# Kernel tuning notes

Hardware: AMD Instinct MI355X
Metric: run time of the kernel (lower is better)

Reference implementation:

```python
import jax, jax.numpy as jnp
import numpy as np

N_NODES = 50000
N_EDGES = 800000
F_IN = 64
F_OUT = 64


def setup_inputs() -> dict:
    key = jax.random.key(0)
    k1, k2, k3, k4, k5 = jax.random.split(key, 5)
    x = jax.random.normal(k1, (N_NODES, F_IN), dtype=jnp.float32)
    edge_index = jax.random.randint(k2, (2, N_EDGES), 0, N_NODES, dtype=jnp.int32)
    # PyG GraphConv params: lin_rel (with bias) applied to aggregated neighbors,
    # lin_root (no bias) applied to the node's own features.
    scale = 1.0 / np.sqrt(F_IN)
    W_rel = jax.random.uniform(k3, (F_OUT, F_IN), dtype=jnp.float32, minval=-scale, maxval=scale)
    b_rel = jax.random.uniform(k4, (F_OUT,), dtype=jnp.float32, minval=-scale, maxval=scale)
    W_root = jax.random.uniform(k5, (F_OUT, F_IN), dtype=jnp.float32, minval=-scale, maxval=scale)
    return {"x": x, "W_rel": W_rel, "b_rel": b_rel, "W_root": W_root, "edge_index": edge_index}


def reference(x, W_rel, b_rel, W_root, edge_index):
    # GraphConv (aggr='add'): out = lin_rel(sum_{j in N(i)} x_j) + lin_root(x_i), then ReLU
    src, dst = edge_index[0], edge_index[1]
    # gather neighbor features along edges, scatter-add into destination nodes
    agg = jax.ops.segment_sum(x[src], dst, num_segments=x.shape[0])  # [N, F_IN]
    out = agg @ W_rel.T + b_rel + x @ W_root.T  # [N, F_OUT]
    return jax.nn.relu(out)
```

## Files before the change

### kernel.cpp

```cpp
#include <hip/hip_runtime.h>


#define FD 64
#define TN 64
#define BC 2048
#define KP 65
#define CS 16
#define TM 1024
#define GB 512

__global__ __launch_bounds__(256) void gcv4_prep(
    const float* __restrict__ W_rel, const float* __restrict__ W_root,
    float* __restrict__ WTrel, float* __restrict__ WTroot,
    int* __restrict__ tcnt, int n_cnt) {
  const int idx = blockIdx.x * 256 + threadIdx.x;
  if (idx < FD * FD) {
    const int o = idx >> 6, k = idx & 63;
    WTrel[k * FD + o] = W_rel[idx];
    WTroot[k * FD + o] = W_root[idx];
  }
  for (int i = idx; i < n_cnt; i += gridDim.x * 256) tcnt[i] = 0;
}

__global__ __launch_bounds__(256) void gcv4_bin(
    const int* __restrict__ eidx, int* __restrict__ tcnt,
    unsigned* __restrict__ tbuf, int n_edges, int n_tiles) {
  __shared__ int hcnt[TM];
  __shared__ int hbase[TM];

  const int t = threadIdx.x;
  for (int i = t; i < n_tiles; i += 256) hcnt[i] = 0;
  __syncthreads();

  const int per = (n_edges + gridDim.x - 1) / gridDim.x;
  const int e0 = blockIdx.x * per;
  const int e1 = min(e0 + per, n_edges);

  for (int e = e0 + t; e < e1; e += 256)
    atomicAdd(&hcnt[eidx[n_edges + e] >> 6], 1);
  __syncthreads();

  for (int i = t; i < n_tiles; i += 256) {
    const int c = hcnt[i];
    hbase[i] = (c > 0) ? atomicAdd(&tcnt[i * CS], c) : 0;
    hcnt[i] = 0;
  }
  __syncthreads();

  for (int e = e0 + t; e < e1; e += 256) {
    const int s = eidx[e];
    const int d = eidx[n_edges + e];
    const int tl = d >> 6;
    const int p = hbase[tl] + atomicAdd(&hcnt[tl], 1);
    if (p < BC)
      tbuf[(size_t)tl * BC + p] = ((unsigned)d << 16) | (unsigned)s;
  }
}

__global__ __launch_bounds__(256) void gcv4_main(
    const float* __restrict__ x,
    const float* __restrict__ WTrel,
    const float* __restrict__ b_rel,
    const float* __restrict__ WTroot,
    const int* __restrict__ tcnt,
    const unsigned* __restrict__ tbuf,
    float* __restrict__ out, int n_nodes) {
  __shared__ float aggT[FD * KP];
  __shared__ unsigned short sl[BC + 64];
  __shared__ int hh[TN];
  __shared__ int oo[TN + 1];
  __shared__ int cc[TN];

  const int t = threadIdx.x;
  const int lane = t & 63;
  const int w = t >> 6;
  const int tile = blockIdx.x;
  const int node0 = tile * TN;
  const int cnt = min(tcnt[tile * CS], BC);
  const unsigned* lst = tbuf + (size_t)tile * BC;

  if (t < TN) hh[t] = 0;
  if (t < 64 && cnt + t < BC + 64) sl[cnt + t] = 0;
  __syncthreads();

  for (int i = t; i < cnt; i += 256) atomicAdd(&hh[(lst[i] >> 16) & 63], 1);
  __syncthreads();

  if (w == 0) {
    int v = hh[lane];
    int s = v;
#pragma unroll
    for (int d = 1; d < 64; d <<= 1) {
      int u = __shfl_up(s, d, 64);
      if (lane >= d) s += u;
    }
    oo[lane] = s - v;
    cc[lane] = s - v;
    if (lane == 63) oo[64] = s;
  }
  __syncthreads();

  for (int i = t; i < cnt; i += 256) {
    const unsigned e = lst[i];
    const int d = (int)((e >> 16) & 63);
    sl[atomicAdd(&cc[d], 1)] = (unsigned short)(e & 0xFFFFu);
  }
  __syncthreads();

  const int slot = lane >> 4;
  const int fq = lane & 15;
  for (int nn = 0; nn < 16; ++nn) {
    const int d = w * 16 + nn;
    const int jb = oo[d];
    const int je = oo[d + 1];
    float4 acc = make_float4(0.f, 0.f, 0.f, 0.f);
    const int i0 = slot, i1 = 4 + slot, i2 = 8 + slot, i3 = 12 + slot;
    for (int e0 = jb; e0 < je; e0 += 16) {
      const int m = je - e0;
      const int j0 = (i0 < m) ? e0 + i0 : cnt;
      const int j1 = (i1 < m) ? e0 + i1 : cnt;
      const int j2 = (i2 < m) ? e0 + i2 : cnt;
      const int j3 = (i3 < m) ? e0 + i3 : cnt;
      const int s0 = (int)sl[j0];
      const int s1 = (int)sl[j1];
      const int s2 = (int)sl[j2];
      const int s3 = (int)sl[j3];
      const float4 f0 = *(const float4*)(x + (size_t)s0 * FD + fq * 4);
      const float4 f1 = *(const float4*)(x + (size_t)s1 * FD + fq * 4);
      const float4 f2 = *(const float4*)(x + (size_t)s2 * FD + fq * 4);
      const float4 f3 = *(const float4*)(x + (size_t)s3 * FD + fq * 4);
      acc.x += (i0 < m ? f0.x : 0.f); acc.y += (i0 < m ? f0.y : 0.f);
      acc.z += (i0 < m ? f0.z : 0.f); acc.w += (i0 < m ? f0.w : 0.f);
      acc.x += (i1 < m ? f1.x : 0.f); acc.y += (i1 < m ? f1.y : 0.f);
      acc.z += (i1 < m ? f1.z : 0.f); acc.w += (i1 < m ? f1.w : 0.f);
      acc.x += (i2 < m ? f2.x : 0.f); acc.y += (i2 < m ? f2.y : 0.f);
      acc.z += (i2 < m ? f2.z : 0.f); acc.w += (i2 < m ? f2.w : 0.f);
      acc.x += (i3 < m ? f3.x : 0.f); acc.y += (i3 < m ? f3.y : 0.f);
      acc.z += (i3 < m ? f3.z : 0.f); acc.w += (i3 < m ? f3.w : 0.f);
    }
    acc.x += __shfl_xor(acc.x, 16, 64); acc.y += __shfl_xor(acc.y, 16, 64);
    acc.z += __shfl_xor(acc.z, 16, 64); acc.w += __shfl_xor(acc.w, 16, 64);
    acc.x += __shfl_xor(acc.x, 32, 64); acc.y += __shfl_xor(acc.y, 32, 64);
    acc.z += __shfl_xor(acc.z, 32, 64); acc.w += __shfl_xor(acc.w, 32, 64);
    if (slot == 0) {
      aggT[(fq * 4 + 0) * KP + d] = acc.x;
      aggT[(fq * 4 + 1) * KP + d] = acc.y;
      aggT[(fq * 4 + 2) * KP + d] = acc.z;
      aggT[(fq * 4 + 3) * KP + d] = acc.w;
    }
  }
  __syncthreads();

  const int oq = t & 15, rq = t >> 4;
  const int o0 = oq * 4, r0 = rq * 4;
  const float* xp0 = x + (size_t)min(node0 + r0 + 0, n_nodes - 1) * FD;
  const float* xp1 = x + (size_t)min(node0 + r0 + 1, n_nodes - 1) * FD;
  const float* xp2 = x + (size_t)min(node0 + r0 + 2, n_nodes - 1) * FD;
  const float* xp3 = x + (size_t)min(node0 + r0 + 3, n_nodes - 1) * FD;
  const float4 bias = *(const float4*)(b_rel + o0);
  float acc[4][4];
#pragma unroll
  for (int ri = 0; ri < 4; ++ri) {
    acc[ri][0] = bias.x; acc[ri][1] = bias.y;
    acc[ri][2] = bias.z; acc[ri][3] = bias.w;
  }
#pragma unroll 2
  for (int k0 = 0; k0 < FD; k0 += 4) {
    const float4 q0 = *(const float4*)(xp0 + k0);
    const float4 q1 = *(const float4*)(xp1 + k0);
    const float4 q2 = *(const float4*)(xp2 + k0);
    const float4 q3 = *(const float4*)(xp3 + k0);
#pragma unroll
    for (int kk = 0; kk < 4; ++kk) {
      const int k = k0 + kk;
      const float4 wr = *(const float4*)(WTrel + k * FD + o0);
      const float4 wo = *(const float4*)(WTroot + k * FD + o0);
      const float a0 = aggT[k * KP + r0 + 0];
      const float a1 = aggT[k * KP + r0 + 1];
      const float a2 = aggT[k * KP + r0 + 2];
      const float a3 = aggT[k * KP + r0 + 3];
      const float x0 = ((const float*)&q0)[kk];
      const float x1 = ((const float*)&q1)[kk];
      const float x2 = ((const float*)&q2)[kk];
      const float x3 = ((const float*)&q3)[kk];
      acc[0][0] += a0 * wr.x + x0 * wo.x; acc[0][1] += a0 * wr.y + x0 * wo.y;
      acc[0][2] += a0 * wr.z + x0 * wo.z; acc[0][3] += a0 * wr.w + x0 * wo.w;
      acc[1][0] += a1 * wr.x + x1 * wo.x; acc[1][1] += a1 * wr.y + x1 * wo.y;
      acc[1][2] += a1 * wr.z + x1 * wo.z; acc[1][3] += a1 * wr.w + x1 * wo.w;
      acc[2][0] += a2 * wr.x + x2 * wo.x; acc[2][1] += a2 * wr.y + x2 * wo.y;
      acc[2][2] += a2 * wr.z + x2 * wo.z; acc[2][3] += a2 * wr.w + x2 * wo.w;
      acc[3][0] += a3 * wr.x + x3 * wo.x; acc[3][1] += a3 * wr.y + x3 * wo.y;
      acc[3][2] += a3 * wr.z + x3 * wo.z; acc[3][3] += a3 * wr.w + x3 * wo.w;
    }
  }
#pragma unroll
  for (int ri = 0; ri < 4; ++ri) {
    const int gi = node0 + r0 + ri;
    if (gi < n_nodes) {
      float4 o4;
      o4.x = fmaxf(acc[ri][0], 0.f); o4.y = fmaxf(acc[ri][1], 0.f);
      o4.z = fmaxf(acc[ri][2], 0.f); o4.w = fmaxf(acc[ri][3], 0.f);
      *(float4*)(out + (size_t)gi * FD + o0) = o4;
    }
  }
}

extern "C" void kernel_launch(void* const* d_in, const int* in_sizes, int n_in,
                              void* d_out, int out_size, void* d_ws, size_t ws_size,
                              hipStream_t stream) {
  const float* x      = (const float*)d_in[0];
  const float* W_rel  = (const float*)d_in[1];
  const float* b_rel  = (const float*)d_in[2];
  const float* W_root = (const float*)d_in[3];
  const int* eidx     = (const int*)d_in[4];

  const int n_nodes = in_sizes[0] / FD;
  const int n_edges = in_sizes[4] / 2;
  const int n_tiles = (n_nodes + TN - 1) / TN;

  int* tcnt      = (int*)d_ws;
  unsigned* tbuf = (unsigned*)(tcnt + (size_t)n_tiles * CS);
  float* WTrel   = (float*)(tbuf + (size_t)n_tiles * BC);
  float* WTroot  = WTrel + FD * FD;

  float* out = (float*)d_out;

  const int n_cnt = n_tiles * CS;
  const int gPrep = (n_cnt + 255) / 256;
  gcv4_prep<<<gPrep, 256, 0, stream>>>(W_rel, W_root, WTrel, WTroot, tcnt,
                                       n_cnt);

  gcv4_bin<<<GB, 256, 0, stream>>>(eidx, tcnt, tbuf, n_edges, n_tiles);

  gcv4_main<<<n_tiles, 256, 0, stream>>>(x, WTrel, b_rel, WTroot, tcnt, tbuf,
                                         out, n_nodes);
}
```

Baseline: 173.9 us.

## Use 512 threads per tile and stage root features in shared memory

The main kernel's block size doubles to 512 threads, so each wavefront aggregates 8 destination nodes instead of 16 and each thread computes 2 output rows instead of 4. The tile's own x rows are loaded coalesced into a transposed shared-memory buffer at the start, replacing strided per-thread global float4 loads in the dense projection. This raises parallelism per tile and removes redundant global reads of x. The cost is more shared memory per block (an extra 64x65 float array), which may limit how many blocks fit per CU.

After: 162.3 us. 6.7% less time.

```diff
diff --git a/kernel.cpp b/kernel.cpp
--- a/kernel.cpp
+++ b/kernel.cpp
@@ -9,7 +9,7 @@
 #define TM 1024
 #define GB 512
 
-__global__ __launch_bounds__(256) void gcv4_prep(
+__global__ __launch_bounds__(256) void gcv5_prep(
     const float* __restrict__ W_rel, const float* __restrict__ W_root,
     float* __restrict__ WTrel, float* __restrict__ WTroot,
     int* __restrict__ tcnt, int n_cnt) {
@@ -22,7 +22,7 @@
   for (int i = idx; i < n_cnt; i += gridDim.x * 256) tcnt[i] = 0;
 }
 
-__global__ __launch_bounds__(256) void gcv4_bin(
+__global__ __launch_bounds__(256) void gcv5_bin(
     const int* __restrict__ eidx, int* __restrict__ tcnt,
     unsigned* __restrict__ tbuf, int n_edges, int n_tiles) {
   __shared__ int hcnt[TM];
@@ -57,7 +57,7 @@
   }
 }
 
-__global__ __launch_bounds__(256) void gcv4_main(
+__global__ __launch_bounds__(512) void gcv5_main(
     const float* __restrict__ x,
     const float* __restrict__ WTrel,
     const float* __restrict__ b_rel,
@@ -66,6 +66,7 @@
     const unsigned* __restrict__ tbuf,
     float* __restrict__ out, int n_nodes) {
   __shared__ float aggT[FD * KP];
+  __shared__ float xT[FD * KP];
   __shared__ unsigned short sl[BC + 64];
   __shared__ int hh[TN];
   __shared__ int oo[TN + 1];
@@ -81,9 +82,24 @@
 
   if (t < TN) hh[t] = 0;
   if (t < 64 && cnt + t < BC + 64) sl[cnt + t] = 0;
-  __syncthreads();
-
-  for (int i = t; i < cnt; i += 256) atomicAdd(&hh[(lst[i] >> 16) & 63], 1);
+  {
+    const int c4 = t & 15;
+    const int rr = t >> 4;
+#pragma unroll
+    for (int p = 0; p < 2; ++p) {
+      const int r = p * 32 + rr;
+      const int gi = node0 + r;
+      float4 v = make_float4(0.f, 0.f, 0.f, 0.f);
+      if (gi < n_nodes) v = *(const float4*)(x + (size_t)gi * FD + c4 * 4);
+      xT[(c4 * 4 + 0) * KP + r] = v.x;
+      xT[(c4 * 4 + 1) * KP + r] = v.y;
+      xT[(c4 * 4 + 2) * KP + r] = v.z;
+      xT[(c4 * 4 + 3) * KP + r] = v.w;
+    }
+  }
+  __syncthreads();
+
+  for (int i = t; i < cnt; i += 512) atomicAdd(&hh[(lst[i] >> 16) & 63], 1);
   __syncthreads();
 
   if (w == 0) {
@@ -100,7 +116,7 @@
   }
   __syncthreads();
 
-  for (int i = t; i < cnt; i += 256) {
+  for (int i = t; i < cnt; i += 512) {
     const unsigned e = lst[i];
     const int d = (int)((e >> 16) & 63);
     sl[atomicAdd(&cc[d], 1)] = (unsigned short)(e & 0xFFFFu);
@@ -109,8 +125,8 @@
 
   const int slot = lane >> 4;
   const int fq = lane & 15;
-  for (int nn = 0; nn < 16; ++nn) {
-    const int d = w * 16 + nn;
+  for (int nn = 0; nn < 8; ++nn) {
+    const int d = w * 8 + nn;
     const int jb = oo[d];
     const int je = oo[d + 1];
     float4 acc = make_float4(0.f, 0.f, 0.f, 0.f);
@@ -152,49 +168,27 @@
   __syncthreads();
 
   const int oq = t & 15, rq = t >> 4;
-  const int o0 = oq * 4, r0 = rq * 4;
-  const float* xp0 = x + (size_t)min(node0 + r0 + 0, n_nodes - 1) * FD;
-  const float* xp1 = x + (size_t)min(node0 + r0 + 1, n_nodes - 1) * FD;
-  const float* xp2 = x + (size_t)min(node0 + r0 + 2, n_nodes - 1) * FD;
-  const float* xp3 = x + (size_t)min(node0 + r0 + 3, n_nodes - 1) * FD;
+  const int o0 = oq * 4, r0 = rq * 2;
   const float4 bias = *(const float4*)(b_rel + o0);
-  float acc[4][4];
-#pragma unroll
-  for (int ri = 0; ri < 4; ++ri) {
+  float acc[2][4];
+#pragma unroll
+  for (int ri = 0; ri < 2; ++ri) {
     acc[ri][0] = bias.x; acc[ri][1] = bias.y;
     acc[ri][2] = bias.z; acc[ri][3] = bias.w;
   }
-#pragma unroll 2
-  for (int k0 = 0; k0 < FD; k0 += 4) {
-    const float4 q0 = *(const float4*)(xp0 + k0);
-    const float4 q1 = *(const float4*)(xp1 + k0);
-    const float4 q2 = *(const float4*)(xp2 + k0);
-    const float4 q3 = *(const float4*)(xp3 + k0);
-#pragma unroll
-    for (int kk = 0; kk < 4; ++kk) {
-      const int k = k0 + kk;
-      const float4 wr = *(const float4*)(WTrel + k * FD + o0);
-      const float4 wo = *(const float4*)(WTroot + k * FD + o0);
-      const float a0 = aggT[k * KP + r0 + 0];
-      const float a1 = aggT[k * KP + r0 + 1];
-      const float a2 = aggT[k * KP + r0 + 2];
-      const float a3 = aggT[k * KP + r0 + 3];
-      const float x0 = ((const float*)&q0)[kk];
-      const float x1 = ((const float*)&q1)[kk];
-      const float x2 = ((const float*)&q2)[kk];
-      const float x3 = ((const float*)&q3)[kk];
-      acc[0][0] += a0 * wr.x + x0 * wo.x; acc[0][1] += a0 * wr.y + x0 * wo.y;
-      acc[0][2] += a0 * wr.z + x0 * wo.z; acc[0][3] += a0 * wr.w + x0 * wo.w;
-      acc[1][0] += a1 * wr.x + x1 * wo.x; acc[1][1] += a1 * wr.y + x1 * wo.y;
-      acc[1][2] += a1 * wr.z + x1 * wo.z; acc[1][3] += a1 * wr.w + x1 * wo.w;
-      acc[2][0] += a2 * wr.x + x2 * wo.x; acc[2][1] += a2 * wr.y + x2 * wo.y;
-      acc[2][2] += a2 * wr.z + x2 * wo.z; acc[2][3] += a2 * wr.w + x2 * wo.w;
-      acc[3][0] += a3 * wr.x + x3 * wo.x; acc[3][1] += a3 * wr.y + x3 * wo.y;
-      acc[3][2] += a3 * wr.z + x3 * wo.z; acc[3][3] += a3 * wr.w + x3 * wo.w;
-    }
-  }
-#pragma unroll
-  for (int ri = 0; ri < 4; ++ri) {
+#pragma unroll 4
+  for (int k = 0; k < FD; ++k) {
+    const float4 wr = *(const float4*)(WTrel + k * FD + o0);
+    const float4 wo = *(const float4*)(WTroot + k * FD + o0);
+    const float a0 = aggT[k * KP + r0 + 0], a1 = aggT[k * KP + r0 + 1];
+    const float x0 = xT[k * KP + r0 + 0], x1 = xT[k * KP + r0 + 1];
+    acc[0][0] += a0 * wr.x + x0 * wo.x; acc[0][1] += a0 * wr.y + x0 * wo.y;
+    acc[0][2] += a0 * wr.z + x0 * wo.z; acc[0][3] += a0 * wr.w + x0 * wo.w;
+    acc[1][0] += a1 * wr.x + x1 * wo.x; acc[1][1] += a1 * wr.y + x1 * wo.y;
+    acc[1][2] += a1 * wr.z + x1 * wo.z; acc[1][3] += a1 * wr.w + x1 * wo.w;
+  }
+#pragma unroll
+  for (int ri = 0; ri < 2; ++ri) {
     const int gi = node0 + r0 + ri;
     if (gi < n_nodes) {
       float4 o4;
@@ -227,11 +221,11 @@
 
   const int n_cnt = n_tiles * CS;
   const int gPrep = (n_cnt + 255) / 256;
-  gcv4_prep<<<gPrep, 256, 0, stream>>>(W_rel, W_root, WTrel, WTroot, tcnt,
+  gcv5_prep<<<gPrep, 256, 0, stream>>>(W_rel, W_root, WTrel, WTroot, tcnt,
                                        n_cnt);
 
-  gcv4_bin<<<GB, 256, 0, stream>>>(eidx, tcnt, tbuf, n_edges, n_tiles);
-
-  gcv4_main<<<n_tiles, 256, 0, stream>>>(x, WTrel, b_rel, WTroot, tcnt, tbuf,
+  gcv5_bin<<<GB, 256, 0, stream>>>(eidx, tcnt, tbuf, n_edges, n_tiles);
+
+  gcv5_main<<<n_tiles, 512, 0, stream>>>(x, WTrel, b_rel, WTroot, tcnt, tbuf,
                                          out, n_nodes);
 }
```
